# Kernel optimization log

Hardware: AMD Instinct MI355X
Metric: run time of the kernel (lower is better)

The kernel has to match this reference:

```python
import jax, jax.numpy as jnp
import numpy as np

NEG = -1e30  # effective -inf, safe under fp32


def setup_inputs() -> dict:
    key = jax.random.key(0)
    k1, k2, k3 = jax.random.split(key, 3)
    T, B, C, L = 2000, 512, 29, 150  # C = num_classes + num_replabels = 28 + 1
    inputs = jax.random.normal(k1, (T, B, C), dtype=jnp.float32)
    transitions = jax.random.normal(k2, (C + 1, C), dtype=jnp.float32) * 0.1
    targets = jax.random.randint(k3, (B, L), 0, C, dtype=jnp.int32)
    return {"inputs": inputs, "transitions": transitions, "targets": targets}


def _asg_loss(inputs, transitions, targets):
    # inputs: [T, B, C] unnormalized emissions (time-major, as fed to the module)
    # transitions: [C+1, C]; row 0 = start scores, transitions[1+c, p] = score(p -> c)
    # targets: [B, L] int labels (replabel-packed), values in [0, C)
    T, B, C = inputs.shape
    L = targets.shape[1]
    start = transitions[0]          # [C]
    trans = transitions[1:]         # [C, C]; trans[next, prev]

    # ---- denominator: log-sum-exp over all paths in the fully connected lattice ----
    alpha0 = inputs[0] + start[None, :]                                   # [B, C]
    def den_step(alpha, e_t):
        # alpha[b, p] -> logsumexp_p(alpha[b, p] + trans[c, p]) per next-class c
        a = jax.nn.logsumexp(alpha[:, None, :] + trans[None, :, :], axis=-1)
        return e_t + a, None
    alphaT, _ = jax.lax.scan(den_step, alpha0, inputs[1:])
    log_den = jax.nn.logsumexp(alphaT, axis=-1)                           # [B]

    # ---- numerator: forced alignment over the target chain with self-loops ----
    idx = jnp.broadcast_to(targets[None, :, :], (T, B, L))
    e_y = jnp.take_along_axis(inputs, idx, axis=2)                        # [T, B, L]
    stay_t = trans[targets, targets]                                      # [B, L] self-loop
    move_t = trans[targets[:, 1:], targets[:, :-1]]                       # [B, L-1] y_{l-1}->y_l
    move_t = jnp.concatenate([jnp.zeros((B, 1), inputs.dtype), move_t], axis=1)
    l_is0 = jnp.arange(L) == 0
    num0 = jnp.where(l_is0[None, :], start[targets[:, 0]][:, None] + e_y[0], NEG)
    def num_step(alpha, e_t):
        shifted = jnp.pad(alpha[:, :-1], ((0, 0), (1, 0)), constant_values=NEG)
        a = jnp.logaddexp(alpha + stay_t, shifted + move_t)
        return e_t + a, None
    alphaL, _ = jax.lax.scan(num_step, num0, e_y[1:])
    log_num = alphaL[:, -1]                                               # [B]

    # loss_b = logZ_full - logZ_forced_align; 'mean' reduction over batch
    return jnp.mean(log_den - log_num)


def reference(inputs, transitions, targets):
    return _asg_loss(inputs, transitions, targets)
```

## Files before the change

kernel.cpp:

```cpp
#include <hip/hip_runtime.h>

static constexpr int Tn = 2000;
static constexpr int Bn = 512;
static constexpr int Cn = 29;
static constexpr int Ln = 150;
static constexpr float LOG2E_F = 1.4426950408889634f;
static constexpr float LN2_F   = 0.6931471805599453f;
static constexpr float NEGV    = -1e30f;

static constexpr int WS_DEN_F = 0;
static constexpr int WS_NUM_F = 2 * 512 * 32;
static constexpr int WS_NUM_B = 2 * 512 * 32 + 512 * 160;

static constexpr int NSEG = 8;
static constexpr int SEGL = 250;

typedef float  f32x16 __attribute__((ext_vector_type(16)));
typedef float  f32x4  __attribute__((ext_vector_type(4)));
typedef __bf16 bf16x8 __attribute__((ext_vector_type(8)));
typedef unsigned int u32x4 __attribute__((ext_vector_type(4)));

#if __has_builtin(__builtin_amdgcn_exp2f)
#define FEXP2(x) __builtin_amdgcn_exp2f(x)
#else
#define FEXP2(x) exp2f(x)
#endif
#if __has_builtin(__builtin_amdgcn_logf)
#define FLOG2(x) __builtin_amdgcn_logf(x)
#else
#define FLOG2(x) log2f(x)
#endif

__device__ __forceinline__ int exp_of(float x) {
    return ((__float_as_int(x) >> 23) & 255) - 127;
}
__device__ __forceinline__ float pow2i(int e) {
    return __int_as_float((e + 127) << 23);
}
__device__ __forceinline__ unsigned short f2bf_rne(float x) {
    unsigned u = __float_as_uint(x);
    u += 0x7fffu + ((u >> 16) & 1u);
    return (unsigned short)(u >> 16);
}
__device__ __forceinline__ unsigned cvtpk_bf16(float lo, float hi) {
    unsigned r;
    asm("v_cvt_pk_bf16_f32 %0, %1, %2" : "=v"(r) : "v"(lo), "v"(hi));
    return r;
}
__device__ __forceinline__ void xswap32(unsigned &a, unsigned &b) {
#if __has_builtin(__builtin_amdgcn_permlane32_swap)
    auto r = __builtin_amdgcn_permlane32_swap(a, b, false, false);
    a = r[0]; b = r[1];
#else
    unsigned pa = (unsigned)__shfl_xor((int)a, 32);
    unsigned pb = (unsigned)__shfl_xor((int)b, 32);
    bool hb = (threadIdx.x & 32) != 0;
    unsigned na = hb ? pb : a;
    unsigned nb = hb ? b : pa;
    a = na; b = nb;
#endif
}
__device__ __forceinline__ void packDtoB(const float* W, bf16x8 &B1, bf16x8 &B2) {
    unsigned pk[8];
#pragma unroll
    for (int q = 0; q < 8; ++q) pk[q] = cvtpk_bf16(W[2 * q], W[2 * q + 1]);
    xswap32(pk[0], pk[2]); xswap32(pk[1], pk[3]);
    xswap32(pk[4], pk[6]); xswap32(pk[5], pk[7]);
    B1 = __builtin_bit_cast(bf16x8, u32x4{pk[0], pk[1], pk[2], pk[3]});
    B2 = __builtin_bit_cast(bf16x8, u32x4{pk[4], pk[5], pk[6], pk[7]});
}
__device__ __forceinline__ void renorm16(float* W, float &Sacc) {
    float m = W[0];
#pragma unroll
    for (int r = 1; r < 16; ++r) m = fmaxf(m, W[r]);
#pragma unroll
    for (int sh = 1; sh <= 32; sh <<= 1) m = fmaxf(m, __shfl_xor(m, sh));
    int g = exp_of(m);
    float iv = pow2i(-g);
#pragma unroll
    for (int r = 0; r < 16; ++r) W[r] *= iv;
    Sacc += (float)g;
}

__global__ __launch_bounds__(512)
void asg_scan(const float* __restrict__ inp, const float* __restrict__ tr,
              const int* __restrict__ tg, float* __restrict__ ws)
{
    const int tid = threadIdx.x;
    const int bid = blockIdx.x;

    __shared__ float mats[NSEG][32][33];
    __shared__ float uring[NSEG][8][32];
    __shared__ float scl[NSEG];

    if (bid >= 128) {
        const int lane = tid & 63;
        const int wid  = tid >> 6;
        const int col  = lane & 31;
        const int hi   = lane >> 5;
        const int b    = bid - 128;
        const size_t BC = (size_t)Bn * Cn;

        unsigned aw[8];
#pragma unroll
        for (int p = 0; p < 8; ++p) {
            int kb = (p >> 2) * 16 + 8 * hi + (p & 3) * 2;
            unsigned short lo = 0, hh = 0;
            if (col < Cn) {
                if (kb < Cn)     lo = f2bf_rne(FEXP2(LOG2E_F * tr[(1 + col) * Cn + kb]));
                if (kb + 1 < Cn) hh = f2bf_rne(FEXP2(LOG2E_F * tr[(1 + col) * Cn + kb + 1]));
            }
            aw[p] = (unsigned)lo | ((unsigned)hh << 16);
        }
        const bf16x8 A1 = __builtin_bit_cast(bf16x8, u32x4{aw[0], aw[1], aw[2], aw[3]});
        const bf16x8 A2 = __builtin_bit_cast(bf16x8, u32x4{aw[4], aw[5], aw[6], aw[7]});

        f32x16 z;
#pragma unroll
        for (int r = 0; r < 16; ++r) z[r] = 0.f;

        const int start = 1 + SEGL * wid;
        const int cnt   = min(SEGL, Tn - start);

        const float* ebase = inp + (size_t)b * Cn + min(col, Cn - 1);

        float er[8];
#pragma unroll
        for (int p = 0; p < 8; ++p)
            er[p] = ebase[(size_t)min(start + p, Tn - 1) * BC];

        if (lane < 32) {
            uring[wid][0][col] = FEXP2(LOG2E_F * er[0]);
            uring[wid][1][col] = FEXP2(LOG2E_F * er[1]);
        }

        float W[16];
#pragma unroll
        for (int r = 0; r < 16; ++r) {
            int row = (r & 3) + 8 * (r >> 2) + 4 * hi;
            W[r] = (row == col) ? 1.0f : 0.0f;
        }
        float Sacc = 0.f;

        int s = 0;
        for (; s + 8 <= cnt; s += 8) {
#pragma unroll
            for (int u = 0; u < 8; ++u) {
                er[u] = ebase[(size_t)min(start + s + u + 8, Tn - 1) * BC];
                float un = FEXP2(LOG2E_F * er[(u + 2) & 7]);
                if (lane < 32) uring[wid][(u + 2) & 7][col] = un;
                f32x4 uu0 = *(const f32x4*)&uring[wid][u][4 * hi];
                f32x4 uu1 = *(const f32x4*)&uring[wid][u][8 + 4 * hi];
                f32x4 uu2 = *(const f32x4*)&uring[wid][u][16 + 4 * hi];
                f32x4 uu3 = *(const f32x4*)&uring[wid][u][24 + 4 * hi];
                bf16x8 B1, B2;
                packDtoB(W, B1, B2);
                f32x16 d = __builtin_amdgcn_mfma_f32_32x32x16_bf16(A1, B1, z, 0, 0, 0);
                d = __builtin_amdgcn_mfma_f32_32x32x16_bf16(A2, B2, d, 0, 0, 0);
#pragma unroll
                for (int r = 0; r < 16; ++r) {
                    f32x4 uq = (r < 4) ? uu0 : (r < 8) ? uu1 : (r < 12) ? uu2 : uu3;
                    W[r] = d[r] * uq[r & 3];
                }
                if (u == 7) renorm16(W, Sacc);
            }
        }
        {
            const int rem = cnt - s;
            if (lane < 32) {
#pragma unroll
                for (int j = 2; j < 8; ++j)
                    if (j < rem) uring[wid][j][col] = FEXP2(LOG2E_F * er[j]);
            }
#pragma unroll
            for (int u = 0; u < 8; ++u) {
                if (u < rem) {
                    f32x4 uu0 = *(const f32x4*)&uring[wid][u][4 * hi];
                    f32x4 uu1 = *(const f32x4*)&uring[wid][u][8 + 4 * hi];
                    f32x4 uu2 = *(const f32x4*)&uring[wid][u][16 + 4 * hi];
                    f32x4 uu3 = *(const f32x4*)&uring[wid][u][24 + 4 * hi];
                    bf16x8 B1, B2;
                    packDtoB(W, B1, B2);
                    f32x16 d = __builtin_amdgcn_mfma_f32_32x32x16_bf16(A1, B1, z, 0, 0, 0);
                    d = __builtin_amdgcn_mfma_f32_32x32x16_bf16(A2, B2, d, 0, 0, 0);
#pragma unroll
                    for (int r = 0; r < 16; ++r) {
                        f32x4 uq = (r < 4) ? uu0 : (r < 8) ? uu1 : (r < 12) ? uu2 : uu3;
                        W[r] = d[r] * uq[r & 3];
                    }
                }
            }
            renorm16(W, Sacc);
        }

#pragma unroll
        for (int r = 0; r < 16; ++r) {
            int row = (r & 3) + 8 * (r >> 2) + 4 * hi;
            mats[wid][row][col] = W[r];
        }
        if (lane == 0) scl[wid] = Sacc;
        __syncthreads();

        auto lds_mul = [&](const float (*Lm)[33], const float (*Rm)[33], float* Wo) {
            unsigned lw[8];
#pragma unroll
            for (int p = 0; p < 8; ++p) {
                int kb = (p >> 2) * 16 + 8 * hi + (p & 3) * 2;
                lw[p] = (unsigned)f2bf_rne(Lm[col][kb]) |
                        ((unsigned)f2bf_rne(Lm[col][kb + 1]) << 16);
            }
            bf16x8 LA1 = __builtin_bit_cast(bf16x8, u32x4{lw[0], lw[1], lw[2], lw[3]});
            bf16x8 LA2 = __builtin_bit_cast(bf16x8, u32x4{lw[4], lw[5], lw[6], lw[7]});
            float Wr[16];
#pragma unroll
            for (int r = 0; r < 16; ++r) {
                int row = (r & 3) + 8 * (r >> 2) + 4 * hi;
                Wr[r] = Rm[row][col];
            }
            bf16x8 B1, B2;
            packDtoB(Wr, B1, B2);
            f32x16 d = __builtin_amdgcn_mfma_f32_32x32x16_bf16(LA1, B1, z, 0, 0, 0);
            d = __builtin_amdgcn_mfma_f32_32x32x16_bf16(LA2, B2, d, 0, 0, 0);
#pragma unroll
            for (int r = 0; r < 16; ++r) Wo[r] = d[r];
        };
        auto store_mat = [&](int slot, const float* Wo) {
#pragma unroll
            for (int r = 0; r < 16; ++r) {
                int row = (r & 3) + 8 * (r >> 2) + 4 * hi;
                mats[slot][row][col] = Wo[r];
            }
        };

        if (wid < 4) {
            float Wq[16];
            lds_mul(mats[2 * wid + 1], mats[2 * wid], Wq);
            float Sg = scl[2 * wid] + scl[2 * wid + 1];
            renorm16(Wq, Sg);
            store_mat(2 * wid, Wq);
            if (lane == 0) scl[2 * wid] = Sg;
        }
        __syncthreads();
        if (wid < 2) {
            float Wq[16];
            lds_mul(mats[4 * wid + 2], mats[4 * wid], Wq);
            float Sg = scl[4 * wid] + scl[4 * wid + 2];
            renorm16(Wq, Sg);
            store_mat(4 * wid, Wq);
            if (lane == 0) scl[4 * wid] = Sg;
        }
        __syncthreads();
        if (wid == 0) {
            float Wq[16];
            lds_mul(mats[4], mats[0], Wq);
            const float Stot = scl[0] + scl[4];
            float a0v = 0.f;
            if (col < Cn)
                a0v = FEXP2(LOG2E_F * (inp[(size_t)b * Cn + col] + tr[col]));
            float ssum = 0.f;
#pragma unroll
            for (int r = 0; r < 16; ++r) ssum += Wq[r];
            float t = ssum * a0v;
#pragma unroll
            for (int sh = 1; sh <= 32; sh <<= 1) t += __shfl_xor(t, sh);
            if (lane == 0) ws[WS_DEN_F + b] = FLOG2(t) + Stot;
        }
    } else {
        const int nid = bid * 8 + (tid >> 6);
        const int dir = nid >> 9;
        const int b   = nid & 511;
        const int k   = tid & 63;
        const int* tb = tg + b * Ln;

        const int l0 = 3 * k, l1 = 3 * k + 1, l2 = 3 * k + 2;
        const int t0i = (l0 < Ln) ? tb[l0] : 0;
        const int t1i = (l1 < Ln) ? tb[l1] : 0;
        const int t2i = (l2 < Ln) ? tb[l2] : 0;
        const float S0 = FEXP2(LOG2E_F * tr[(1 + t0i) * Cn + t0i]);
        const float S1 = FEXP2(LOG2E_F * tr[(1 + t1i) * Cn + t1i]);
        const float S2 = FEXP2(LOG2E_F * tr[(1 + t2i) * Cn + t2i]);
        const float M0 = (l0 >= 1 && l0 < Ln)
                         ? FEXP2(LOG2E_F * tr[(1 + t0i) * Cn + tb[l0 - 1]]) : 0.f;
        const float M1 = (l1 < Ln) ? FEXP2(LOG2E_F * tr[(1 + t1i) * Cn + t0i]) : 0.f;
        const float M2 = (l2 < Ln) ? FEXP2(LOG2E_F * tr[(1 + t2i) * Cn + t1i]) : 0.f;

        float w0 = 0.f, w1 = 0.f, w2 = 0.f;
        if (dir == 0) {
            if (k == 0) w0 = FEXP2(LOG2E_F * (tr[t0i] + inp[(size_t)b * Cn + t0i]));
        } else {
            if (k == 49) w2 = 1.f;
        }
        int   sE  = 0;
        float m0x = M0;
        float fdn = 1.f;
        int   pgx = 0, psp = 0;

        const size_t BC = (size_t)Bn * Cn;
        const int o0 = b * Cn + t0i, o1 = b * Cn + t1i, o2 = b * Cn + t2i;
        const int t0 = dir ? (Tn - 1) : 1;
        const int dt = dir ? -1 : 1;
        const int steps = dir ? 1000 : 999;

        float ue0[4], ue1[4], ue2[4], nr0[4], nr1[4], nr2[4];
#pragma unroll
        for (int u = 0; u < 4; ++u) {
            const float* pt = inp + (size_t)(t0 + u * dt) * BC;
            ue0[u] = FEXP2(LOG2E_F * pt[o0]);
            ue1[u] = FEXP2(LOG2E_F * pt[o1]);
            ue2[u] = FEXP2(LOG2E_F * pt[o2]);
        }

        for (int s = 0; s < steps; s += 4) {
#pragma unroll
            for (int u = 0; u < 4; ++u) {
                const float* pt = inp + (size_t)(t0 + (s + 4 + u) * dt) * BC;
                nr0[u] = pt[o0]; nr1[u] = pt[o1]; nr2[u] = pt[o2];
            }
#pragma unroll
            for (int u = 0; u < 4; ++u) {
                if (s + u < steps) {
                    if (u == 1) {
                        float rs = pow2i(-pgx);
                        w0 *= rs; w1 *= rs; w2 *= rs; sE += pgx;
                        int df = psp - sE;
                        df = max(-126, min(56, df));
                        float fx = pow2i(df);
                        m0x = M0 * fx; fdn = fx;
                    }
                    if (dir == 0) {
                        float sh = __shfl_up(w2, 1);
                        sh = (k == 0) ? 0.f : sh;
                        float n0 = ue0[u] * fmaf(w0, S0, sh * m0x);
                        float n1 = ue1[u] * fmaf(w1, S1, w0 * M1);
                        float n2 = ue2[u] * fmaf(w2, S2, w1 * M2);
                        w0 = n0; w1 = n1; w2 = n2;
                    } else {
                        float q0 = w0 * ue0[u], q1 = w1 * ue1[u], q2 = w2 * ue2[u];
                        float mn = __shfl_down(q0 * M0, 1);
                        w0 = fmaf(q0, S0, q1 * M1);
                        w1 = fmaf(q1, S1, q2 * M2);
                        w2 = fmaf(q2, S2, mn * fdn);
                    }
                    if (u == 3) {
                        float mxn = fmaxf(fmaxf(w0, w1), w2);
                        pgx = (mxn > 0.f) ? exp_of(mxn) : 0;
                        int sp = sE + pgx;
                        psp = dir ? __shfl_down(sp, 1) : __shfl_up(sp, 1);
                    }
                }
            }
#pragma unroll
            for (int u = 0; u < 4; ++u) {
                ue0[u] = FEXP2(LOG2E_F * nr0[u]);
                ue1[u] = FEXP2(LOG2E_F * nr1[u]);
                ue2[u] = FEXP2(LOG2E_F * nr2[u]);
            }
        }
        const float fsE = (float)sE;
        const int base = (dir ? WS_NUM_B : WS_NUM_F) + b * 160;
        if (l0 < Ln)     ws[base + l0]     = (w0 > 0.f) ? FLOG2(w0) + fsE : NEGV;
        if (l0 + 1 < Ln) ws[base + l0 + 1] = (w1 > 0.f) ? FLOG2(w1) + fsE : NEGV;
        if (l0 + 2 < Ln) ws[base + l0 + 2] = (w2 > 0.f) ? FLOG2(w2) + fsE : NEGV;
    }
}

__global__ __launch_bounds__(512)
void asg_combine(const float* __restrict__ ws, float* __restrict__ out)
{
    __shared__ float red[512];
    const int b = threadIdx.x;

    const float ld = ws[WS_DEN_F + b];

    const float* nf = ws + WS_NUM_F + b * 160;
    const float* nb = ws + WS_NUM_B + b * 160;
    float vm2 = -3.0e38f;
    for (int l = 0; l < Ln; ++l) vm2 = fmaxf(vm2, nf[l] + nb[l]);
    float sum2 = 0.f;
    for (int l = 0; l < Ln; ++l) sum2 += FEXP2(nf[l] + nb[l] - vm2);
    float ln = vm2 + FLOG2(sum2);

    red[b] = ld - ln;
    __syncthreads();
    for (int off = 256; off > 0; off >>= 1) {
        if (b < off) red[b] += red[b + off];
        __syncthreads();
    }
    if (b == 0) out[0] = red[0] * (LN2_F / 512.0f);
}

extern "C" void kernel_launch(void* const* d_in, const int* in_sizes, int n_in,
                              void* d_out, int out_size, void* d_ws, size_t ws_size,
                              hipStream_t stream)
{
    const float* inp = (const float*)d_in[0];
    const float* tr  = (const float*)d_in[1];
    const int*   tg  = (const int*)d_in[2];
    float* out = (float*)d_out;
    float* ws  = (float*)d_ws;

    hipLaunchKernelGGL(asg_scan,    dim3(640), dim3(512), 0, stream, inp, tr, tg, ws);
    hipLaunchKernelGGL(asg_combine, dim3(1),   dim3(512), 0, stream, ws, out);
}
```

Before: 253.3 us.

## Deepen emission prefetch, store LDS matrices as bf16, reorder block roles

Both the denominator MFMA scan and the numerator chain scan now prefetch emissions two groups ahead through rotating register buffers. The goal is to hide global-load latency behind the serial recurrence. The segment-product matrices are now kept in LDS as pre-packed bf16, so the tree reduction loads MFMA operands with vector reads instead of converting floats one by one. Denominator blocks now take the low block indices and numerator blocks follow them, and the tail loop is trimmed to the two leftover steps. The cost is extra register pressure from the deeper buffers.

```diff
diff --git a/kernel.cpp b/kernel.cpp
--- a/kernel.cpp
+++ b/kernel.cpp
@@ -89,16 +89,16 @@
     const int tid = threadIdx.x;
     const int bid = blockIdx.x;
 
-    __shared__ float mats[NSEG][32][33];
+    __shared__ unsigned am[NSEG][32][20];
     __shared__ float uring[NSEG][8][32];
     __shared__ float scl[NSEG];
 
-    if (bid >= 128) {
+    if (bid < 512) {
         const int lane = tid & 63;
         const int wid  = tid >> 6;
         const int col  = lane & 31;
         const int hi   = lane >> 5;
-        const int b    = bid - 128;
+        const int b    = bid;
         const size_t BC = (size_t)Bn * Cn;
 
         unsigned aw[8];
@@ -124,15 +124,19 @@
 
         const float* ebase = inp + (size_t)b * Cn + min(col, Cn - 1);
 
-        float er[8];
-#pragma unroll
-        for (int p = 0; p < 8; ++p)
-            er[p] = ebase[(size_t)min(start + p, Tn - 1) * BC];
-
-        if (lane < 32) {
-            uring[wid][0][col] = FEXP2(LOG2E_F * er[0]);
-            uring[wid][1][col] = FEXP2(LOG2E_F * er[1]);
-        }
+        {
+            float r0 = ebase[(size_t)(start)     * BC];
+            float r1 = ebase[(size_t)(start + 1) * BC];
+            if (lane < 32) {
+                uring[wid][0][col] = FEXP2(LOG2E_F * r0);
+                uring[wid][1][col] = FEXP2(LOG2E_F * r1);
+            }
+        }
+        float er[8], er2[8];
+#pragma unroll
+        for (int u = 0; u < 8; ++u) er[u]  = ebase[(size_t)(start + 2 + u) * BC];
+#pragma unroll
+        for (int u = 0; u < 8; ++u) er2[u] = ebase[(size_t)(start + 10 + u) * BC];
 
         float W[16];
 #pragma unroll
@@ -144,10 +148,11 @@
 
         int s = 0;
         for (; s + 8 <= cnt; s += 8) {
+            float nl[8];
 #pragma unroll
             for (int u = 0; u < 8; ++u) {
-                er[u] = ebase[(size_t)min(start + s + u + 8, Tn - 1) * BC];
-                float un = FEXP2(LOG2E_F * er[(u + 2) & 7]);
+                nl[u] = ebase[(size_t)min(start + s + 18 + u, Tn - 1) * BC];
+                float un = FEXP2(LOG2E_F * er[u]);
                 if (lane < 32) uring[wid][(u + 2) & 7][col] = un;
                 f32x4 uu0 = *(const f32x4*)&uring[wid][u][4 * hi];
                 f32x4 uu1 = *(const f32x4*)&uring[wid][u][8 + 4 * hi];
@@ -164,16 +169,13 @@
                 }
                 if (u == 7) renorm16(W, Sacc);
             }
+#pragma unroll
+            for (int u = 0; u < 8; ++u) { er[u] = er2[u]; er2[u] = nl[u]; }
         }
         {
             const int rem = cnt - s;
-            if (lane < 32) {
-#pragma unroll
-                for (int j = 2; j < 8; ++j)
-                    if (j < rem) uring[wid][j][col] = FEXP2(LOG2E_F * er[j]);
-            }
-#pragma unroll
-            for (int u = 0; u < 8; ++u) {
+#pragma unroll
+            for (int u = 0; u < 2; ++u) {
                 if (u < rem) {
                     f32x4 uu0 = *(const f32x4*)&uring[wid][u][4 * hi];
                     f32x4 uu1 = *(const f32x4*)&uring[wid][u][8 + 4 * hi];
@@ -193,48 +195,51 @@
             renorm16(W, Sacc);
         }
 
-#pragma unroll
-        for (int r = 0; r < 16; ++r) {
-            int row = (r & 3) + 8 * (r >> 2) + 4 * hi;
-            mats[wid][row][col] = W[r];
+        {
+            unsigned short* s16 = (unsigned short*)am[wid];
+#pragma unroll
+            for (int r = 0; r < 16; ++r) {
+                int row = (r & 3) + 8 * (r >> 2) + 4 * hi;
+                s16[row * 40 + col] = f2bf_rne(W[r]);
+            }
         }
         if (lane == 0) scl[wid] = Sacc;
         __syncthreads();
 
-        auto lds_mul = [&](const float (*Lm)[33], const float (*Rm)[33], float* Wo) {
-            unsigned lw[8];
-#pragma unroll
-            for (int p = 0; p < 8; ++p) {
-                int kb = (p >> 2) * 16 + 8 * hi + (p & 3) * 2;
-                lw[p] = (unsigned)f2bf_rne(Lm[col][kb]) |
-                        ((unsigned)f2bf_rne(Lm[col][kb + 1]) << 16);
-            }
-            bf16x8 LA1 = __builtin_bit_cast(bf16x8, u32x4{lw[0], lw[1], lw[2], lw[3]});
-            bf16x8 LA2 = __builtin_bit_cast(bf16x8, u32x4{lw[4], lw[5], lw[6], lw[7]});
-            float Wr[16];
-#pragma unroll
-            for (int r = 0; r < 16; ++r) {
-                int row = (r & 3) + 8 * (r >> 2) + 4 * hi;
-                Wr[r] = Rm[row][col];
-            }
-            bf16x8 B1, B2;
-            packDtoB(Wr, B1, B2);
+        auto lds_mul = [&](int Ls, int Rs, float* Wo) {
+            u32x4 a0 = *(const u32x4*)&am[Ls][col][4 * hi];
+            u32x4 a1 = *(const u32x4*)&am[Ls][col][8 + 4 * hi];
+            bf16x8 LA1 = __builtin_bit_cast(bf16x8, a0);
+            bf16x8 LA2 = __builtin_bit_cast(bf16x8, a1);
+            const unsigned short* r16 = (const unsigned short*)am[Rs];
+            unsigned pk[8];
+#pragma unroll
+            for (int q = 0; q < 8; ++q) {
+                int ra = ((2 * q) & 3) + 8 * ((2 * q) >> 2) + 4 * hi;
+                pk[q] = (unsigned)r16[ra * 40 + col] |
+                        ((unsigned)r16[(ra + 1) * 40 + col] << 16);
+            }
+            xswap32(pk[0], pk[2]); xswap32(pk[1], pk[3]);
+            xswap32(pk[4], pk[6]); xswap32(pk[5], pk[7]);
+            bf16x8 B1 = __builtin_bit_cast(bf16x8, u32x4{pk[0], pk[1], pk[2], pk[3]});
+            bf16x8 B2 = __builtin_bit_cast(bf16x8, u32x4{pk[4], pk[5], pk[6], pk[7]});
             f32x16 d = __builtin_amdgcn_mfma_f32_32x32x16_bf16(LA1, B1, z, 0, 0, 0);
             d = __builtin_amdgcn_mfma_f32_32x32x16_bf16(LA2, B2, d, 0, 0, 0);
 #pragma unroll
             for (int r = 0; r < 16; ++r) Wo[r] = d[r];
         };
         auto store_mat = [&](int slot, const float* Wo) {
+            unsigned short* s16 = (unsigned short*)am[slot];
 #pragma unroll
             for (int r = 0; r < 16; ++r) {
                 int row = (r & 3) + 8 * (r >> 2) + 4 * hi;
-                mats[slot][row][col] = Wo[r];
+                s16[row * 40 + col] = f2bf_rne(Wo[r]);
             }
         };
 
         if (wid < 4) {
             float Wq[16];
-            lds_mul(mats[2 * wid + 1], mats[2 * wid], Wq);
+            lds_mul(2 * wid + 1, 2 * wid, Wq);
             float Sg = scl[2 * wid] + scl[2 * wid + 1];
             renorm16(Wq, Sg);
             store_mat(2 * wid, Wq);
@@ -243,7 +248,7 @@
         __syncthreads();
         if (wid < 2) {
             float Wq[16];
-            lds_mul(mats[4 * wid + 2], mats[4 * wid], Wq);
+            lds_mul(4 * wid + 2, 4 * wid, Wq);
             float Sg = scl[4 * wid] + scl[4 * wid + 2];
             renorm16(Wq, Sg);
             store_mat(4 * wid, Wq);
@@ -252,7 +257,7 @@
         __syncthreads();
         if (wid == 0) {
             float Wq[16];
-            lds_mul(mats[4], mats[0], Wq);
+            lds_mul(4, 0, Wq);
             const float Stot = scl[0] + scl[4];
             float a0v = 0.f;
             if (col < Cn)
@@ -266,7 +271,7 @@
             if (lane == 0) ws[WS_DEN_F + b] = FLOG2(t) + Stot;
         }
     } else {
-        const int nid = bid * 8 + (tid >> 6);
+        const int nid = (bid - 512) * 8 + (tid >> 6);
         const int dir = nid >> 9;
         const int b   = nid & 511;
         const int k   = tid & 63;
@@ -301,7 +306,7 @@
         const int dt = dir ? -1 : 1;
         const int steps = dir ? 1000 : 999;
 
-        float ue0[4], ue1[4], ue2[4], nr0[4], nr1[4], nr2[4];
+        float ue0[4], ue1[4], ue2[4], pr0[4], pr1[4], pr2[4];
 #pragma unroll
         for (int u = 0; u < 4; ++u) {
             const float* pt = inp + (size_t)(t0 + u * dt) * BC;
@@ -309,12 +314,18 @@
             ue1[u] = FEXP2(LOG2E_F * pt[o1]);
             ue2[u] = FEXP2(LOG2E_F * pt[o2]);
         }
+#pragma unroll
+        for (int u = 0; u < 4; ++u) {
+            const float* pt = inp + (size_t)(t0 + (4 + u) * dt) * BC;
+            pr0[u] = pt[o0]; pr1[u] = pt[o1]; pr2[u] = pt[o2];
+        }
 
         for (int s = 0; s < steps; s += 4) {
+            float n0[4], n1[4], n2[4];
 #pragma unroll
             for (int u = 0; u < 4; ++u) {
-                const float* pt = inp + (size_t)(t0 + (s + 4 + u) * dt) * BC;
-                nr0[u] = pt[o0]; nr1[u] = pt[o1]; nr2[u] = pt[o2];
+                const float* pt = inp + (size_t)(t0 + (s + 8 + u) * dt) * BC;
+                n0[u] = pt[o0]; n1[u] = pt[o1]; n2[u] = pt[o2];
             }
 #pragma unroll
             for (int u = 0; u < 4; ++u) {
@@ -330,10 +341,10 @@
                     if (dir == 0) {
                         float sh = __shfl_up(w2, 1);
                         sh = (k == 0) ? 0.f : sh;
-                        float n0 = ue0[u] * fmaf(w0, S0, sh * m0x);
-                        float n1 = ue1[u] * fmaf(w1, S1, w0 * M1);
-                        float n2 = ue2[u] * fmaf(w2, S2, w1 * M2);
-                        w0 = n0; w1 = n1; w2 = n2;
+                        float nn0 = ue0[u] * fmaf(w0, S0, sh * m0x);
+                        float nn1 = ue1[u] * fmaf(w1, S1, w0 * M1);
+                        float nn2 = ue2[u] * fmaf(w2, S2, w1 * M2);
+                        w0 = nn0; w1 = nn1; w2 = nn2;
                     } else {
                         float q0 = w0 * ue0[u], q1 = w1 * ue1[u], q2 = w2 * ue2[u];
                         float mn = __shfl_down(q0 * M0, 1);
@@ -351,9 +362,10 @@
             }
 #pragma unroll
             for (int u = 0; u < 4; ++u) {
-                ue0[u] = FEXP2(LOG2E_F * nr0[u]);
-                ue1[u] = FEXP2(LOG2E_F * nr1[u]);
-                ue2[u] = FEXP2(LOG2E_F * nr2[u]);
+                ue0[u] = FEXP2(LOG2E_F * pr0[u]);
+                ue1[u] = FEXP2(LOG2E_F * pr1[u]);
+                ue2[u] = FEXP2(LOG2E_F * pr2[u]);
+                pr0[u] = n0[u]; pr1[u] = n1[u]; pr2[u] = n2[u];
             }
         }
         const float fsE = (float)sE;
```

After: 327.1 us. +29.2%, slower.
